# Kernel optimization log

Measured on AMD Instinct MI355X. Metric: run time of the kernel, lower is better.

The kernel has to match this reference:

```python
import jax, jax.numpy as jnp
import numpy as np

N_NODES = 50000
N_EDGES = 800000
N_FEAT = 512
HIDDEN = 128
N_CLASSES = 32


def spmm(edge_src, edge_dst, edge_val, dense):
    # A @ dense where A is COO: A[edge_src, edge_dst] = edge_val
    msgs = edge_val[:, None] * dense[edge_dst]          # [E, D]
    return jax.ops.segment_sum(msgs, edge_src, num_segments=N_NODES)


def setup_inputs() -> dict:
    key = jax.random.key(0)
    ks = jax.random.split(key, 6)
    x = jax.random.normal(ks[0], (N_NODES, N_FEAT), dtype=jnp.float32)
    edge_src = jax.random.randint(ks[1], (N_EDGES,), 0, N_NODES, dtype=jnp.int32)
    edge_dst = jax.random.randint(ks[2], (N_EDGES,), 0, N_NODES, dtype=jnp.int32)
    edge_val = jax.random.uniform(ks[3], (N_EDGES,), dtype=jnp.float32)
    # glorot init as in the original
    lim1 = np.sqrt(6.0 / (N_FEAT + HIDDEN))
    lim2 = np.sqrt(6.0 / (HIDDEN + N_CLASSES))
    W1 = jax.random.uniform(ks[4], (N_FEAT, HIDDEN), minval=-lim1, maxval=lim1, dtype=jnp.float32)
    W2 = jax.random.uniform(ks[5], (HIDDEN, N_CLASSES), minval=-lim2, maxval=lim2, dtype=jnp.float32)
    return {"x": x, "edge_src": edge_src, "edge_dst": edge_dst,
            "edge_val": edge_val, "W1": W1, "W2": W2}


def reference(x, edge_src, edge_dst, edge_val, W1, W2):
    # Layer 1: relu(A @ (X @ W1))  (dropout=0 at inference)
    pre1 = x @ W1                                        # [N, H]
    h = jax.nn.relu(spmm(edge_src, edge_dst, edge_val, pre1))
    # Layer 2 (output, identity activation): A @ (H @ W2)
    pre2 = h @ W2                                        # [N, C]
    out = spmm(edge_src, edge_dst, edge_val, pre2)
    return out
```

## Files before the change

### kernel.cpp

```cpp
#include <hip/hip_runtime.h>
#include <hip/hip_bf16.h>

#define N_NODES 50000
#define N_EDGES 800000
#define N_FEAT 512
#define HIDDEN 128
#define N_CLASSES 32

#define NBUCK 196
#define REG_STRIDE 6144
#define NCHUNK 7

typedef __attribute__((ext_vector_type(8))) short bf16x8;
typedef __attribute__((ext_vector_type(4))) float f32x4;

static __device__ __forceinline__ unsigned short f2bf(float f) {
    unsigned u = __float_as_uint(f);
    u += 0x7FFFu + ((u >> 16) & 1u);
    return (unsigned short)(u >> 16);
}
static __device__ __forceinline__ float bflo(unsigned u) { return __uint_as_float(u << 16); }
static __device__ __forceinline__ float bfhi(unsigned u) { return __uint_as_float(u & 0xFFFF0000u); }
static __device__ __forceinline__ unsigned pack2(float a, float b) {
    union { __hip_bfloat162 h; unsigned u; } c;
    c.h = __float22bfloat162_rn(make_float2(a, b));
    return c.u;
}


__global__ __launch_bounds__(256) void bucket1_k(const int* __restrict__ src, const int* __restrict__ dst,
                                                 const float* __restrict__ val,
                                                 int* __restrict__ gcursor,
                                                 unsigned long long* __restrict__ tmp) {
    __shared__ int cnt[256];
    __shared__ int lstart[256];
    __shared__ int lcur[256];
    __shared__ int gbase[256];
    __shared__ unsigned long long buf[2048];
    const int t = threadIdx.x;
    const int e0 = blockIdx.x * 2048;
    const int ne = min(2048, N_EDGES - e0);

    cnt[t] = 0;
    __syncthreads();

    unsigned long long rec[8];
    int rb[8];
#pragma unroll
    for (int j = 0; j < 8; ++j) {
        int p = j * 256 + t;
        rec[j] = 0; rb[j] = -1;
        if (p < ne) {
            int i = e0 + p;
            unsigned s = (unsigned)src[i];
            rec[j] = (unsigned long long)(s | ((unsigned)dst[i] << 16))
                   | ((unsigned long long)__float_as_uint(val[i]) << 32);
            int b = (int)(s >> 8);
            rb[j] = b;
            atomicAdd(&cnt[b], 1);
        }
    }
    __syncthreads();
    const int cv = cnt[t];
    for (int off = 1; off < 256; off <<= 1) {
        int xv = (t >= off) ? cnt[t - off] : 0;
        __syncthreads();
        cnt[t] += xv;
        __syncthreads();
    }
    lstart[t] = cnt[t] - cv;
    lcur[t]   = cnt[t] - cv;
    if (t < NBUCK) gbase[t] = atomicAdd(&gcursor[t], cv);
    __syncthreads();
#pragma unroll
    for (int j = 0; j < 8; ++j) {
        if (rb[j] >= 0) {
            int pos = atomicAdd(&lcur[rb[j]], 1);
            buf[pos] = rec[j];
        }
    }
    __syncthreads();
#pragma unroll
    for (int j = 0; j < 8; ++j) {
        int p = j * 256 + t;
        if (p < ne) {
            unsigned long long r = buf[p];
            int b = (int)((r & 0xFFFFu) >> 8);
            int tgt = gbase[b] + (p - lstart[b]);
            tmp[(size_t)b * REG_STRIDE + tgt] = r;
        }
    }
}


__global__ __launch_bounds__(256) void bucket2_k(const int* __restrict__ gcursor,
                                                 const unsigned long long* __restrict__ tmp,
                                                 unsigned long long* __restrict__ csr_ev,
                                                 int* __restrict__ row_ptr) {
    __shared__ int lcnt[256 * NCHUNK];
    __shared__ int lcur[256 * NCHUNK];
    __shared__ int rowsum[256];
    __shared__ int cnts[NBUCK];
    __shared__ int base_s;
    const int b = blockIdx.x;
    const int t = threadIdx.x;
    if (t < NBUCK) cnts[t] = gcursor[t];
    for (int j = t; j < 256 * NCHUNK; j += 256) lcnt[j] = 0;
    __syncthreads();
    const int nb = cnts[b];
    if (t == 0) {
        int s = 0;
        for (int r = 0; r < b; ++r) s += cnts[r];
        base_s = s;
    }
    const unsigned long long* reg = tmp + (size_t)b * REG_STRIDE;
    __syncthreads();
    for (int p = t; p < nb; p += 256) {
        unsigned long long r = reg[p];
        int n = (int)(r & 0xFFu);
        int ch = (int)(((r >> 16) & 0xFFFFu) >> 13);
        atomicAdd(&lcnt[n * NCHUNK + ch], 1);
    }
    __syncthreads();
    int rs = 0;
#pragma unroll
    for (int c = 0; c < NCHUNK; ++c) rs += lcnt[t * NCHUNK + c];
    rowsum[t] = rs;
    __syncthreads();
    for (int off = 1; off < 256; off <<= 1) {
        int xv = (t >= off) ? rowsum[t - off] : 0;
        __syncthreads();
        rowsum[t] += xv;
        __syncthreads();
    }
    const int start = base_s + rowsum[t] - rs;
    int o = start;
#pragma unroll
    for (int c = 0; c < NCHUNK; ++c) { lcur[t * NCHUNK + c] = o; o += lcnt[t * NCHUNK + c]; }
    int node = b * 256 + t;
    if (node <= N_NODES) row_ptr[node] = start;
    __syncthreads();
    for (int p = t; p < nb; p += 256) {
        unsigned long long r = reg[p];
        int n = (int)(r & 0xFFu);
        int ch = (int)(((r >> 16) & 0xFFFFu) >> 13);
        int pos = atomicAdd(&lcur[n * NCHUNK + ch], 1);
        csr_ev[pos] = ((r >> 16) & 0xFFFFull) | (r & 0xFFFFFFFF00000000ull);
    }
}


__global__ __launch_bounds__(256) void w1conv_k(const float* __restrict__ W1,
                                                unsigned short* __restrict__ W1t,
                                                int* __restrict__ gcursor) {
    if (blockIdx.x == 0 && threadIdx.x < NBUCK) gcursor[threadIdx.x] = 0;
    int id = blockIdx.x * 256 + threadIdx.x;
    int c = id >> 9;
    int k = id & 511;
    W1t[(size_t)c * N_FEAT + k] = f2bf(W1[(size_t)k * HIDDEN + c]);
}


__global__ __launch_bounds__(1024, 1) void gemm1_mfma(const float* __restrict__ x,
                                                      const unsigned short* __restrict__ W1t,
                                                      unsigned short* __restrict__ pre1b) {
    __shared__ char lds[131072];

    const int t = threadIdx.x;
    const int w = t >> 6;
    const int l = t & 63;
    const int l15 = l & 15;
    const int lhi = l >> 4;

#pragma unroll
    for (int j = 0; j < 8; ++j) {
        int c = w * 8 + j;
        int n = c & 7, ks = c >> 3;
        int col = n * 16 + l15;
        int k = ks * 32 + lhi * 8;
        __builtin_amdgcn_global_load_lds(W1t + (size_t)col * N_FEAT + k,
                                         (unsigned short*)(lds + c * 1024), 16, 0, 0);
    }
    __syncthreads();

    const int g = w * 256 + blockIdx.x;
    if (g >= N_NODES / 16) return;

    const float* xr = x + (size_t)(g * 16 + l15) * N_FEAT + lhi * 8;

    f32x4 acc[8];
#pragma unroll
    for (int n = 0; n < 8; ++n) acc[n] = (f32x4){0.f, 0.f, 0.f, 0.f};

    float4 qa[3], qb[3];
#pragma unroll
    for (int j = 0; j < 3; ++j) {
        qa[j] = *(const float4*)(xr + j * 32);
        qb[j] = *(const float4*)(xr + j * 32 + 4);
    }
#pragma unroll
    for (int ks = 0; ks < 16; ++ks) {
        float4 c0 = qa[ks % 3], c1 = qb[ks % 3];
        if (ks + 3 < 16) {
            qa[ks % 3] = *(const float4*)(xr + (ks + 3) * 32);
            qb[ks % 3] = *(const float4*)(xr + (ks + 3) * 32 + 4);
        }
        union { bf16x8 v; __hip_bfloat162 h[4]; } u;
        u.h[0] = __float22bfloat162_rn(make_float2(c0.x, c0.y));
        u.h[1] = __float22bfloat162_rn(make_float2(c0.z, c0.w));
        u.h[2] = __float22bfloat162_rn(make_float2(c1.x, c1.y));
        u.h[3] = __float22bfloat162_rn(make_float2(c1.z, c1.w));
        const char* bp = lds + (ks * 8) * 1024 + l * 16;
        __builtin_amdgcn_s_setprio(1);
#pragma unroll
        for (int n = 0; n < 8; ++n) {
            bf16x8 bf = *(const bf16x8*)(bp + n * 1024);
            acc[n] = __builtin_amdgcn_mfma_f32_16x16x32_bf16(u.v, bf, acc[n], 0, 0, 0);
        }
        __builtin_amdgcn_s_setprio(0);
    }
    unsigned short* orow = pre1b + (size_t)(g * 16 + lhi * 4) * HIDDEN + l15;
#pragma unroll
    for (int n = 0; n < 8; ++n)
#pragma unroll
        for (int j = 0; j < 4; ++j)
            orow[(size_t)j * HIDDEN + n * 16] = f2bf(acc[n][j]);
}


__global__ __launch_bounds__(256) void spmm1_k(const int* __restrict__ rp,
                                               const unsigned long long* __restrict__ ce,
                                               const unsigned* __restrict__ P,
                                               unsigned* __restrict__ hb) {
    const int g = threadIdx.x >> 6;
    const int lane = threadIdx.x & 63;
    const int node = blockIdx.x * 4 + g;
    if (node >= N_NODES) return;
    const int s = rp[node], e = rp[node + 1];
    float2 a0, a1, a2, a3;
    a0.x = a0.y = a1.x = a1.y = 0.f;
    a2.x = a2.y = a3.x = a3.y = 0.f;
    int i = s;
    for (; i + 4 <= e; i += 4) {
        unsigned long long e0 = ce[i],     e1 = ce[i + 1];
        unsigned long long e2 = ce[i + 2], e3 = ce[i + 3];
        unsigned u0 = P[(size_t)(unsigned)e0 * 64 + lane];
        unsigned u1 = P[(size_t)(unsigned)e1 * 64 + lane];
        unsigned u2 = P[(size_t)(unsigned)e2 * 64 + lane];
        unsigned u3 = P[(size_t)(unsigned)e3 * 64 + lane];
        float v0 = __uint_as_float((unsigned)(e0 >> 32));
        float v1 = __uint_as_float((unsigned)(e1 >> 32));
        float v2 = __uint_as_float((unsigned)(e2 >> 32));
        float v3 = __uint_as_float((unsigned)(e3 >> 32));
        a0.x += v0 * bflo(u0); a0.y += v0 * bfhi(u0);
        a1.x += v1 * bflo(u1); a1.y += v1 * bfhi(u1);
        a2.x += v2 * bflo(u2); a2.y += v2 * bfhi(u2);
        a3.x += v3 * bflo(u3); a3.y += v3 * bfhi(u3);
    }
    for (; i < e; ++i) {
        unsigned long long e0 = ce[i];
        unsigned u0 = P[(size_t)(unsigned)e0 * 64 + lane];
        float v0 = __uint_as_float((unsigned)(e0 >> 32));
        a0.x += v0 * bflo(u0); a0.y += v0 * bfhi(u0);
    }
    a0.x += a1.x + a2.x + a3.x;
    a0.y += a1.y + a2.y + a3.y;
    a0.x = a0.x > 0.f ? a0.x : 0.f;
    a0.y = a0.y > 0.f ? a0.y : 0.f;
    hb[(size_t)node * 64 + lane] = pack2(a0.x, a0.y);
}


__global__ __launch_bounds__(256) void gemm2_k(const unsigned* __restrict__ hb,
                                               const float* __restrict__ W2,
                                               unsigned short* __restrict__ pre2b) {
    __shared__ float hs[32][132];
    __shared__ float w2s[HIDDEN][N_CLASSES];
    const int t = threadIdx.x;
    const int row0 = blockIdx.x * 32;
#pragma unroll
    for (int j = 0; j < 4; ++j) {
        int f = j * 256 + t;
        int r = f >> 3;
        int c = (f & 7) << 2;
        *(float4*)&w2s[r][c] = *(const float4*)(W2 + (size_t)r * N_CLASSES + c);
    }
#pragma unroll
    for (int j = 0; j < 2; ++j) {
        int f = j * 256 + t;
        int r = f >> 4;
        int cu = (f & 15) << 2;
        int grr = row0 + r;
        if (grr >= N_NODES) grr = N_NODES - 1;
        uint4 u = *(const uint4*)(hb + (size_t)grr * 64 + cu);
        hs[r][2 * cu + 0] = bflo(u.x); hs[r][2 * cu + 1] = bfhi(u.x);
        hs[r][2 * cu + 2] = bflo(u.y); hs[r][2 * cu + 3] = bfhi(u.y);
        hs[r][2 * cu + 4] = bflo(u.z); hs[r][2 * cu + 5] = bfhi(u.z);
        hs[r][2 * cu + 6] = bflo(u.w); hs[r][2 * cu + 7] = bfhi(u.w);
    }
    __syncthreads();
    const int r = t >> 3;
    const int c = (t & 7) << 2;
    float4 acc; acc.x = acc.y = acc.z = acc.w = 0.f;
#pragma unroll 16
    for (int kk = 0; kk < HIDDEN; ++kk) {
        float a = hs[r][kk];
        float4 b = *(const float4*)&w2s[kk][c];
        acc.x += a * b.x; acc.y += a * b.y; acc.z += a * b.z; acc.w += a * b.w;
    }
    int grr = row0 + r;
    if (grr < N_NODES) {
        uint2 o;
        o.x = pack2(acc.x, acc.y);
        o.y = pack2(acc.z, acc.w);
        *(uint2*)&pre2b[(size_t)grr * N_CLASSES + c] = o;
    }
}


__global__ __launch_bounds__(256) void spmm2_k(const int* __restrict__ rp,
                                               const unsigned long long* __restrict__ ce,
                                               const unsigned* __restrict__ P2,
                                               float* __restrict__ out) {
    const int g = threadIdx.x >> 6;
    const int lane = threadIdx.x & 63;
    const int node = blockIdx.x * 4 + g;
    if (node >= N_NODES) return;
    const int s = rp[node], e = rp[node + 1];
    const int f2 = lane & 15;
    const int par = lane >> 4;
    float ax0 = 0.f, ay0 = 0.f, ax1 = 0.f, ay1 = 0.f;
    int i = s + par;
    for (; i + 4 < e; i += 8) {
        unsigned long long e0 = ce[i], e1 = ce[i + 4];
        unsigned u0 = P2[(size_t)(unsigned)e0 * 16 + f2];
        unsigned u1 = P2[(size_t)(unsigned)e1 * 16 + f2];
        float v0 = __uint_as_float((unsigned)(e0 >> 32));
        float v1 = __uint_as_float((unsigned)(e1 >> 32));
        ax0 += v0 * bflo(u0); ay0 += v0 * bfhi(u0);
        ax1 += v1 * bflo(u1); ay1 += v1 * bfhi(u1);
    }
    if (i < e) {
        unsigned long long e0 = ce[i];
        unsigned u0 = P2[(size_t)(unsigned)e0 * 16 + f2];
        float v0 = __uint_as_float((unsigned)(e0 >> 32));
        ax0 += v0 * bflo(u0); ay0 += v0 * bfhi(u0);
    }
    float ax = ax0 + ax1, ay = ay0 + ay1;
    ax += __shfl_xor(ax, 16); ay += __shfl_xor(ay, 16);
    ax += __shfl_xor(ax, 32); ay += __shfl_xor(ay, 32);
    if (lane < 16) {
        float2 o; o.x = ax; o.y = ay;
        ((float2*)out)[(size_t)node * 16 + f2] = o;
    }
}


extern "C" void kernel_launch(void* const* d_in, const int* in_sizes, int n_in,
                              void* d_out, int out_size, void* d_ws, size_t ws_size,
                              hipStream_t stream) {
    const float* x    = (const float*)d_in[0];
    const int* esrc   = (const int*)d_in[1];
    const int* edst   = (const int*)d_in[2];
    const float* ev   = (const float*)d_in[3];
    const float* W1   = (const float*)d_in[4];
    const float* W2   = (const float*)d_in[5];
    float* out        = (float*)d_out;

    unsigned short* pre1b = (unsigned short*)d_ws;
    unsigned* hb          = (unsigned*)(pre1b + 6400000);
    unsigned short* pre2b = pre1b;
    unsigned long long* csr_ev = (unsigned long long*)(hb + 3200000);
    unsigned long long* tmp    = csr_ev + 800000;
    int* row_ptr          = (int*)(tmp + (size_t)NBUCK * REG_STRIDE);
    int* gcursor          = row_ptr + 50048;
    unsigned short* W1t   = (unsigned short*)(gcursor + 256);

    hipLaunchKernelGGL(w1conv_k,   dim3(256),  dim3(256), 0, stream, W1, W1t, gcursor);
    hipLaunchKernelGGL(bucket1_k,  dim3(391),  dim3(256), 0, stream, esrc, edst, ev, gcursor, tmp);
    hipLaunchKernelGGL(bucket2_k,  dim3(NBUCK),dim3(256), 0, stream, gcursor, tmp, csr_ev, row_ptr);

    hipLaunchKernelGGL(gemm1_mfma, dim3(256),  dim3(1024), 0, stream, x, W1t, pre1b);
    hipLaunchKernelGGL(spmm1_k,    dim3(12500),dim3(256), 0, stream, row_ptr, csr_ev, (const unsigned*)pre1b, hb);
    hipLaunchKernelGGL(gemm2_k,    dim3(1563), dim3(256), 0, stream, hb, W2, pre2b);
    hipLaunchKernelGGL(spmm2_k,    dim3(12500),dim3(256), 0, stream, row_ptr, csr_ev, (const unsigned*)pre2b, out);
}
```

Before: 131.8 us.

## Fuse second GEMM into first SpMM epilogue via wave shuffles

```diff
diff --git a/kernel.cpp b/kernel.cpp
--- a/kernel.cpp
+++ b/kernel.cpp
@@ -228,14 +228,23 @@
 }
 
 
-__global__ __launch_bounds__(256) void spmm1_k(const int* __restrict__ rp,
-                                               const unsigned long long* __restrict__ ce,
-                                               const unsigned* __restrict__ P,
-                                               unsigned* __restrict__ hb) {
-    const int g = threadIdx.x >> 6;
-    const int lane = threadIdx.x & 63;
+__global__ __launch_bounds__(256) void spmm1g2_k(const int* __restrict__ rp,
+                                                 const unsigned long long* __restrict__ ce,
+                                                 const unsigned* __restrict__ P,
+                                                 const float* __restrict__ W2,
+                                                 unsigned* __restrict__ pre2b) {
+    __shared__ float w2s[HIDDEN * N_CLASSES];
+    const int t = threadIdx.x;
+#pragma unroll
+    for (int j = 0; j < 4; ++j) {
+        int f = j * 256 + t;
+        *(float4*)&w2s[f * 4] = *(const float4*)(W2 + f * 4);
+    }
+    __syncthreads();
+
+    const int g = t >> 6;
+    const int lane = t & 63;
     const int node = blockIdx.x * 4 + g;
-    if (node >= N_NODES) return;
     const int s = rp[node], e = rp[node + 1];
     float2 a0, a1, a2, a3;
     a0.x = a0.y = a1.x = a1.y = 0.f;
@@ -267,54 +276,22 @@
     a0.y += a1.y + a2.y + a3.y;
     a0.x = a0.x > 0.f ? a0.x : 0.f;
     a0.y = a0.y > 0.f ? a0.y : 0.f;
-    hb[(size_t)node * 64 + lane] = pack2(a0.x, a0.y);
-}
-
-
-__global__ __launch_bounds__(256) void gemm2_k(const unsigned* __restrict__ hb,
-                                               const float* __restrict__ W2,
-                                               unsigned short* __restrict__ pre2b) {
-    __shared__ float hs[32][132];
-    __shared__ float w2s[HIDDEN][N_CLASSES];
-    const int t = threadIdx.x;
-    const int row0 = blockIdx.x * 32;
-#pragma unroll
-    for (int j = 0; j < 4; ++j) {
-        int f = j * 256 + t;
-        int r = f >> 3;
-        int c = (f & 7) << 2;
-        *(float4*)&w2s[r][c] = *(const float4*)(W2 + (size_t)r * N_CLASSES + c);
-    }
-#pragma unroll
-    for (int j = 0; j < 2; ++j) {
-        int f = j * 256 + t;
-        int r = f >> 4;
-        int cu = (f & 15) << 2;
-        int grr = row0 + r;
-        if (grr >= N_NODES) grr = N_NODES - 1;
-        uint4 u = *(const uint4*)(hb + (size_t)grr * 64 + cu);
-        hs[r][2 * cu + 0] = bflo(u.x); hs[r][2 * cu + 1] = bfhi(u.x);
-        hs[r][2 * cu + 2] = bflo(u.y); hs[r][2 * cu + 3] = bfhi(u.y);
-        hs[r][2 * cu + 4] = bflo(u.z); hs[r][2 * cu + 5] = bfhi(u.z);
-        hs[r][2 * cu + 6] = bflo(u.w); hs[r][2 * cu + 7] = bfhi(u.w);
-    }
-    __syncthreads();
-    const int r = t >> 3;
-    const int c = (t & 7) << 2;
-    float4 acc; acc.x = acc.y = acc.z = acc.w = 0.f;
-#pragma unroll 16
-    for (int kk = 0; kk < HIDDEN; ++kk) {
-        float a = hs[r][kk];
-        float4 b = *(const float4*)&w2s[kk][c];
-        acc.x += a * b.x; acc.y += a * b.y; acc.z += a * b.z; acc.w += a * b.w;
-    }
-    int grr = row0 + r;
-    if (grr < N_NODES) {
-        uint2 o;
-        o.x = pack2(acc.x, acc.y);
-        o.y = pack2(acc.z, acc.w);
-        *(uint2*)&pre2b[(size_t)grr * N_CLASSES + c] = o;
-    }
+
+    const int c = lane & 31;
+    const int base = (lane >> 5) * 32;
+    float acc2 = 0.f;
+#pragma unroll
+    for (int kk = 0; kk < 32; ++kk) {
+        int src = base + kk;
+        float hx = __shfl(a0.x, src);
+        float hy = __shfl(a0.y, src);
+        acc2 += hx * w2s[(2 * src) * N_CLASSES + c] + hy * w2s[(2 * src + 1) * N_CLASSES + c];
+    }
+    acc2 += __shfl_xor(acc2, 32);
+    const int f2 = lane & 15;
+    float v0 = __shfl(acc2, 2 * f2);
+    float v1 = __shfl(acc2, 2 * f2 + 1);
+    if (lane < 16) pre2b[(size_t)node * 16 + f2] = pack2(v0, v1);
 }
 
 
@@ -368,9 +345,8 @@
     float* out        = (float*)d_out;
 
     unsigned short* pre1b = (unsigned short*)d_ws;
-    unsigned* hb          = (unsigned*)(pre1b + 6400000);
-    unsigned short* pre2b = pre1b;
-    unsigned long long* csr_ev = (unsigned long long*)(hb + 3200000);
+    unsigned* pre2b       = (unsigned*)(pre1b + 6400000);
+    unsigned long long* csr_ev = (unsigned long long*)((char*)d_ws + 26 * 1024 * 1024);
     unsigned long long* tmp    = csr_ev + 800000;
     int* row_ptr          = (int*)(tmp + (size_t)NBUCK * REG_STRIDE);
     int* gcursor          = row_ptr + 50048;
@@ -381,7 +357,8 @@
     hipLaunchKernelGGL(bucket2_k,  dim3(NBUCK),dim3(256), 0, stream, gcursor, tmp, csr_ev, row_ptr);
 
     hipLaunchKernelGGL(gemm1_mfma, dim3(256),  dim3(1024), 0, stream, x, W1t, pre1b);
-    hipLaunchKernelGGL(spmm1_k,    dim3(12500),dim3(256), 0, stream, row_ptr, csr_ev, (const unsigned*)pre1b, hb);
-    hipLaunchKernelGGL(gemm2_k,    dim3(1563), dim3(256), 0, stream, hb, W2, pre2b);
-    hipLaunchKernelGGL(spmm2_k,    dim3(12500),dim3(256), 0, stream, row_ptr, csr_ev, (const unsigned*)pre2b, out);
-}
+    hipLaunchKernelGGL(spmm1g2_k,  dim3(12500),dim3(256), 0, stream, row_ptr, csr_ev,
+                       (const unsigned*)pre1b, W2, pre2b);
+    hipLaunchKernelGGL(spmm2_k,    dim3(12500),dim3(256), 0, stream, row_ptr, csr_ev,
+                       (const unsigned*)pre2b, out);
+}
```

After: 149.3 us. 13.3% more time.
